# Optimization experiments

Hardware: AMD Instinct MI355X
Metric: run time of the kernel (lower is better)

## Reference

```python
import jax, jax.numpy as jnp
import numpy as np

P_TOP = 0.1          # fraction of brightest pixels for atmosphere
LEC_K = 3            # local-extremum conv kernel size (w=3 in forward)
HID = 64             # hidden channels of stand-in Net


def _conv2d(x, w, pad):
    return jax.lax.conv_general_dilated(
        x, w, window_strides=(1, 1), padding=[(pad, pad), (pad, pad)],
        dimension_numbers=("NCHW", "OIHW", "NCHW"))


def _lec_weights(k, dtype):
    # LocalExtremumConv.init_weights: all +/-1/k^2 with +/-1 at the center
    base = jnp.full((1, 1, k, k), 1.0 / (k * k), dtype=dtype)
    base = base.at[0, 0, k // 2, k // 2].set(1.0)
    return -base, base  # (min_weights, max_weights)


def setup_inputs() -> dict:
    key = jax.random.key(0)
    ks = jax.random.split(key, 8)
    B, C, H, W = 8, 3, 512, 512
    x = jax.random.uniform(ks[0], (B, C, H, W), dtype=jnp.float32)
    s1 = 1.0 / np.sqrt(C * 9)
    s2 = 1.0 / np.sqrt(HID * 9)
    return {
        "x": x,
        "net_w1": jax.random.normal(ks[1], (HID, C, 3, 3), jnp.float32) * s1,
        "net_b1": jnp.zeros((HID,), jnp.float32),
        "net_w2": jax.random.normal(ks[2], (C, HID, 3, 3), jnp.float32) * s2,
        "net_b2": jnp.zeros((C,), jnp.float32),
        "color_w": jax.random.normal(ks[3], (3, 3), jnp.float32) * (1.0 / np.sqrt(3)),
        "color_b": jnp.zeros((3,), jnp.float32),
        "conv_w": jax.random.normal(ks[4], (4, 3, 1, 1), jnp.float32) * (1.0 / np.sqrt(3)),
        "conv_b": jnp.zeros((4,), jnp.float32),
    }


def reference(x, net_w1, net_b1, net_w2, net_b2, color_w, color_b, conv_w, conv_b):
    B, C, H, W = x.shape
    # --- stand-in Net: 3->64->3 conv enhancement, sigmoid output ---
    h = jax.nn.relu(_conv2d(x, net_w1, 1) + net_b1[None, :, None, None])
    img_high = jax.nn.sigmoid(_conv2d(h, net_w2, 1) + net_b2[None, :, None, None])
    # --- stand-in Color_pred: GAP -> linear -> sigmoid -> (B,3,1,1) gain ---
    color = jax.nn.sigmoid(x.mean(axis=(2, 3)) @ color_w.T + color_b)
    img_high = img_high * color[:, :, None, None]
    # --- 1x1 conv -> split K (1ch), Bias (3ch); residual correction ---
    feat = _conv2d(img_high, conv_w, 0) + conv_b[None, :, None, None]
    K, Bt = feat[:, 0:1], feat[:, 1:4]
    x_out = K * x - Bt + x
    # --- illumination channel: reflect pad + channel min/max + LEC convs ---
    pad = LEC_K // 2
    xp = jnp.pad(x_out, ((0, 0), (0, 0), (pad, pad), (pad, pad)), mode="reflect")
    x_max = xp.max(axis=1, keepdims=True)
    _, max_w = _lec_weights(LEC_K, x.dtype)
    bright = jax.nn.relu(_conv2d(x_max, max_w, 0))  # (B,1,H,W)
    # --- atmosphere: top-p% brightest pixels, gather + mean ---
    # NOTE: faithful to torch images.view(B,-1,C) on NCHW (layout-scrambled)
    flat_img = x_out.reshape(B, H * W, C)
    flat_bright = bright.reshape(B, H * W)
    num_pixels = int(P_TOP * H * W)
    _, idx = jax.lax.top_k(flat_bright, num_pixels)          # (B, num_pixels)
    picked = jnp.take_along_axis(flat_img, idx[:, :, None], axis=1)
    A = picked.mean(axis=1)                                   # (B, C)
    return (x_out, A)
```

## Files before the change

### kernel.cpp

```cpp
#include <hip/hip_runtime.h>
#include <hip/hip_bf16.h>

#define Hn 512
#define Wn 512
#define HWn (512 * 512)
#define KTOP 26214

#define HBS 70
#define HBROW (18 * HBS)

typedef __attribute__((ext_vector_type(8))) short frag_ab;
typedef __attribute__((ext_vector_type(4))) float frag_cd;

__device__ __forceinline__ float sigf(float z) { return 1.0f / (1.0f + __expf(-z)); }

__device__ __forceinline__ short f2bf(float f) {
  unsigned u = __float_as_uint(f);
  u += 0x7FFFu + ((u >> 16) & 1u);
  return (short)(u >> 16);
}

__device__ __forceinline__ unsigned aload(const unsigned* p) {
  return __hip_atomic_load(p, __ATOMIC_RELAXED, __HIP_MEMORY_SCOPE_AGENT);
}

__global__ __launch_bounds__(256) void k_means(
    const float* __restrict__ x, float* __restrict__ means, unsigned* __restrict__ doneCnt,
    const float* __restrict__ w1, const float* __restrict__ b1, const float* __restrict__ w2,
    const float* __restrict__ cw, const float* __restrict__ cb,
    short* __restrict__ w1A, short* __restrict__ w2A, int* __restrict__ kbTab,
    float* __restrict__ colorG)
{
  const int tid = threadIdx.x;
  __shared__ int lastS;
  int bc = blockIdx.x >> 5;
  int slice = blockIdx.x & 31;
  const float4* p = (const float4*)(x + bc * HWn + slice * 8192);
  float s = 0.f;
  for (int i = tid; i < 2048; i += 256) { float4 v = p[i]; s += v.x + v.y + v.z + v.w; }
  for (int off = 32; off > 0; off >>= 1) s += __shfl_down(s, off);
  if ((tid & 63) == 0) atomicAdd(&means[bc], s);
  __syncthreads();
  if (tid == 0) {
    unsigned tk = __hip_atomic_fetch_add(doneCnt, 1u, __ATOMIC_RELAXED, __HIP_MEMORY_SCOPE_AGENT);
    lastS = (tk == 767);
  }
  __syncthreads();
  if (!lastS) return;

  {
    int chunk = tid >> 6, lane = tid & 63;
    int m = lane & 15, q = lane >> 4;
    for (int j = 0; j < 8; ++j) {
      int k = q * 8 + j;
      float v = (k < 27) ? w1[(chunk * 16 + m) * 27 + k] : 0.f;
      w1A[tid * 8 + j] = f2bf(v);
    }
  }
  if (tid < 64) {
    int q = tid >> 4;
    for (int j = 0; j < 8; ++j) {
      int k = q * 8 + j;
      int kk = (k < 27) ? k : (k - 27);
      int ic = kk / 9; int r = kk - ic * 9;
      kbTab[tid * 8 + j] = (ic * 240 + (r / 3) * 20 + (r % 3)) * 2;
    }
  }
  for (int i = tid; i < 384; i += 256) {
    int step = i >> 6, lane = i & 63;
    int m = lane & 15, q = lane >> 4;
    int dx = step >> 1, half = step & 1;
    int dy = m / 3, oc = m - dy * 3;
    for (int j = 0; j < 8; ++j) {
      int ch = half * 32 + q * 8 + j;
      float v = (m < 9) ? w2[oc * 576 + ch * 9 + dy * 3 + dx] : 0.f;
      w2A[i * 8 + j] = f2bf(v);
    }
  }
  if (tid < 24) {
    int b = tid / 3, oc = tid % 3;
    float z = cb[oc];
    for (int j = 0; j < 3; ++j)
      z += (atomicAdd(&means[b * 3 + j], 0.f) * (1.0f / (float)HWn)) * cw[oc * 3 + j];
    colorG[tid] = sigf(z);
  }
}

__global__ __launch_bounds__(256, 6) void k_fused(
    const float* __restrict__ x, const float* __restrict__ b1,
    const float* __restrict__ b2, const float* __restrict__ convw, const float* __restrict__ convb,
    const short* __restrict__ w1Ag, const short* __restrict__ w2Ag,
    const int* __restrict__ kbTab,
    const float* __restrict__ colorG, float* __restrict__ out, float* __restrict__ Mb)
{
  __shared__ __align__(16) unsigned short xs[720];
  __shared__ __align__(16) unsigned short hb[180 * HBS];
  __shared__ float bs[64];
  __shared__ float b2s[3], colorS[3], cwS[12], cbS[4];

  const int tid = threadIdx.x;
  const int wid = tid >> 6, lane = tid & 63;
  const int n = lane & 15, q = lane >> 4;
  const int tx0 = blockIdx.x * 16, ty0 = blockIdx.y * 8;
  const int b = blockIdx.z;
  const bool inter = (blockIdx.x - 1u) < 30u && (blockIdx.y - 1u) < 62u;

  if (tid < 180) {
    int c = tid / 60, rem = tid - c * 60;
    int yy = rem / 5, xq = (rem - yy * 5) * 4;
    int gy = ty0 - 2 + yy, gx0 = tx0 - 2 + xq;
    const float* rp = x + (b * 3 + c) * HWn + (gy << 9) + gx0;
    float v0, v1, v2, v3;
    if (inter) {
      v0 = rp[0]; v1 = rp[1]; v2 = rp[2]; v3 = rp[3];
    } else {
      bool rowok = (unsigned)gy < 512u;
      v0 = (rowok && (unsigned)(gx0 + 0) < 512u) ? rp[0] : 0.f;
      v1 = (rowok && (unsigned)(gx0 + 1) < 512u) ? rp[1] : 0.f;
      v2 = (rowok && (unsigned)(gx0 + 2) < 512u) ? rp[2] : 0.f;
      v3 = (rowok && (unsigned)(gx0 + 3) < 512u) ? rp[3] : 0.f;
    }
    __hip_bfloat162 c01 = __float22bfloat162_rn(make_float2(v0, v1));
    __hip_bfloat162 c23 = __float22bfloat162_rn(make_float2(v2, v3));
    uint2 v2w; v2w.x = *(unsigned*)&c01; v2w.y = *(unsigned*)&c23;
    *(uint2*)(xs + c * 240 + yy * 20 + xq) = v2w;
  }
  if (tid < 64) bs[tid] = b1[tid];
  if (tid < 3)  b2s[tid] = b2[tid];
  if (tid < 3)  colorS[tid] = colorG[b * 3 + tid];
  if (tid < 12) cwS[tid] = convw[tid];
  if (tid < 4)  cbS[tid] = convb[tid];

  frag_ab w1f[4];
#pragma unroll
  for (int ck = 0; ck < 4; ++ck) w1f[ck] = *(const frag_ab*)(w1Ag + (ck * 64 + lane) * 8);

  int kb[8];
  {
    const int4* kp = (const int4*)(kbTab + lane * 8);
    int4 ka = kp[0], kc = kp[1];
    kb[0] = ka.x; kb[1] = ka.y; kb[2] = ka.z; kb[3] = ka.w;
    kb[4] = kc.x; kb[5] = kc.y; kb[6] = kc.z; kb[7] = kc.w;
  }
  __syncthreads();

  float biasr[4][4];
#pragma unroll
  for (int ck = 0; ck < 4; ++ck)
#pragma unroll
    for (int r = 0; r < 4; ++r) biasr[ck][r] = bs[ck * 16 + q * 4 + r];

  if (inter) {
    for (int g = wid; g < 12; g += 4) {
      int pt = g * 16 + n;
      int ptc = (pt < 180) ? pt : 179;
      int pty = (ptc * 3641) >> 16;
      int ptx = ptc - pty * 18;
      int baseB = (pty * 20 + ptx) * 2;
      frag_ab B;
#pragma unroll
      for (int j = 0; j < 8; ++j)
        B[j] = *(const short*)((const char*)xs + baseB + kb[j]);
#pragma unroll
      for (int ck = 0; ck < 4; ++ck) {
        frag_cd D = {biasr[ck][0], biasr[ck][1], biasr[ck][2], biasr[ck][3]};
        D = __builtin_amdgcn_mfma_f32_16x16x32_bf16(w1f[ck], B, D, 0, 0, 0);
        float2 p01 = make_float2(fmaxf(D[0], 0.f), fmaxf(D[1], 0.f));
        float2 p23 = make_float2(fmaxf(D[2], 0.f), fmaxf(D[3], 0.f));
        __hip_bfloat162 c01 = __float22bfloat162_rn(p01);
        __hip_bfloat162 c23 = __float22bfloat162_rn(p23);
        uint2 v2; v2.x = *(unsigned*)&c01; v2.y = *(unsigned*)&c23;
        *(uint2*)(hb + ptc * HBS + ck * 16 + q * 4) = v2;
      }
    }
  } else {
    for (int g = wid; g < 12; g += 4) {
      int pt = g * 16 + n;
      int ptc = (pt < 180) ? pt : 179;
      int pty = (ptc * 3641) >> 16;
      int ptx = ptc - pty * 18;
      int baseB = (pty * 20 + ptx) * 2;
      int gy = ty0 - 1 + pty, gx = tx0 - 1 + ptx;
      bool valid = (unsigned)gy < 512u && (unsigned)gx < 512u;
      frag_ab B;
#pragma unroll
      for (int j = 0; j < 8; ++j)
        B[j] = *(const short*)((const char*)xs + baseB + kb[j]);
#pragma unroll
      for (int ck = 0; ck < 4; ++ck) {
        frag_cd D = {biasr[ck][0], biasr[ck][1], biasr[ck][2], biasr[ck][3]};
        D = __builtin_amdgcn_mfma_f32_16x16x32_bf16(w1f[ck], B, D, 0, 0, 0);
        float2 p01 = make_float2(fmaxf(D[0], 0.f), fmaxf(D[1], 0.f));
        float2 p23 = make_float2(fmaxf(D[2], 0.f), fmaxf(D[3], 0.f));
        __hip_bfloat162 c01 = __float22bfloat162_rn(p01);
        __hip_bfloat162 c23 = __float22bfloat162_rn(p23);
        unsigned lo = valid ? *(unsigned*)&c01 : 0u;
        unsigned hi = valid ? *(unsigned*)&c23 : 0u;
        uint2 v2; v2.x = lo; v2.y = hi;
        *(uint2*)(hb + ptc * HBS + ck * 16 + q * 4) = v2;
      }
    }
  }

  frag_ab w2f[6];
#pragma unroll
  for (int i = 0; i < 6; ++i) w2f[i] = *(const frag_ab*)(w2Ag + (i * 64 + lane) * 8);
  __syncthreads();

  for (int r = wid; r < 10; r += 4) {
    frag_cd acc = {0.f, 0.f, 0.f, 0.f};
#pragma unroll
    for (int i = 0; i < 6; ++i) {
      int dx = i >> 1;
      int chb = (i & 1) * 64 + q * 16;
      frag_ab Bf = *(const frag_ab*)((const char*)hb + (r * 18 + n + dx) * (HBS * 2) + chb);
      acc = __builtin_amdgcn_mfma_f32_16x16x32_bf16(w2f[i], Bf, acc, 0, 0, 0);
    }
    float* dp = (float*)(hb + r * HBROW) + n * 10 + q * 4;
    if (q < 2) {
      *(float2*)dp = make_float2(acc[0], acc[1]);
      *(float2*)(dp + 2) = make_float2(acc[2], acc[3]);
    } else if (q == 2) {
      dp[0] = acc[0];
    }
  }
  __syncthreads();

  if (tid < 128) {
    int y = tid >> 4, xcol = tid & 15;
    float a0 = b2s[0], a1 = b2s[1], a2 = b2s[2];
#pragma unroll
    for (int dy = 0; dy < 3; ++dy) {
      const float* dp = (const float*)(hb + (y + dy) * HBROW) + xcol * 10 + dy * 3;
      a0 += dp[0]; a1 += dp[1]; a2 += dp[2];
    }
    float ih0 = colorS[0] * sigf(a0);
    float ih1 = colorS[1] * sigf(a1);
    float ih2 = colorS[2] * sigf(a2);
    float Kv = cwS[0] * ih0 + cwS[1]  * ih1 + cwS[2]  * ih2 + cbS[0];
    float f1 = cwS[3] * ih0 + cwS[4]  * ih1 + cwS[5]  * ih2 + cbS[1];
    float f2 = cwS[6] * ih0 + cwS[7]  * ih1 + cwS[8]  * ih2 + cbS[2];
    float f3 = cwS[9] * ih0 + cwS[10] * ih1 + cwS[11] * ih2 + cbS[3];
    float xc0 = __bfloat162float(*(const __hip_bfloat16*)&xs[0 * 240 + (y + 2) * 20 + (xcol + 2)]);
    float xc1 = __bfloat162float(*(const __hip_bfloat16*)&xs[1 * 240 + (y + 2) * 20 + (xcol + 2)]);
    float xc2 = __bfloat162float(*(const __hip_bfloat16*)&xs[2 * 240 + (y + 2) * 20 + (xcol + 2)]);
    int oi = ((ty0 + y) << 9) + (tx0 + xcol);
    float o0 = Kv * xc0 - f1 + xc0;
    float o1 = Kv * xc1 - f2 + xc1;
    float o2 = Kv * xc2 - f3 + xc2;
    out[(b * 3 + 0) * HWn + oi] = o0;
    out[(b * 3 + 1) * HWn + oi] = o1;
    out[(b * 3 + 2) * HWn + oi] = o2;
    Mb[b * HWn + oi] = fmaxf(fmaxf(o0, o1), o2);
  }
}

__device__ __forceinline__ void softBarrier(unsigned* ctr, unsigned target) {
  __syncthreads();
  if (threadIdx.x == 0) {
    __hip_atomic_fetch_add(ctr, 1u, __ATOMIC_RELAXED, __HIP_MEMORY_SCOPE_AGENT);
    while (__hip_atomic_load(ctr, __ATOMIC_RELAXED, __HIP_MEMORY_SCOPE_AGENT) < target)
      __builtin_amdgcn_s_sleep(2);
  }
  __syncthreads();
}

__device__ void sel256(const unsigned* __restrict__ h, unsigned kneed,
                       unsigned* sm, unsigned* oBin, unsigned* oAbove)
{
  const int t = threadIdx.x;
  sm[t] = aload(&h[t]);
  __syncthreads();
  for (int d = 1; d < 256; d <<= 1) {
    unsigned add = (t + d < 256) ? sm[t + d] : 0u;
    __syncthreads();
    sm[t] += add;
    __syncthreads();
  }
  unsigned mine = sm[t];
  unsigned nxt = (t < 255) ? sm[t + 1] : 0u;
  if (mine >= kneed && nxt < kneed) { *oBin = (unsigned)t; *oAbove = nxt; }
  __syncthreads();
}

__device__ void sel4096(const unsigned* __restrict__ h, unsigned kneed,
                        unsigned* sm, unsigned* oBin, unsigned* oAbove)
{
  const int t = threadIdx.x;
  unsigned loc[16]; unsigned sum = 0;
#pragma unroll
  for (int i = 0; i < 16; ++i) { loc[i] = aload(&h[t * 16 + i]); sum += loc[i]; }
  sm[t] = sum;
  __syncthreads();
  for (int d = 1; d < 256; d <<= 1) {
    unsigned add = (t + d < 256) ? sm[t + d] : 0u;
    __syncthreads();
    sm[t] += add;
    __syncthreads();
  }
  unsigned mine = sm[t];
  unsigned nxt = (t < 255) ? sm[t + 1] : 0u;
  if (mine >= kneed && nxt < kneed) {
    unsigned acc = nxt;
    for (int i = 15; i >= 0; --i) {
      unsigned c = loc[i];
      if (acc + c >= kneed) { *oBin = (unsigned)(t * 16 + i); *oAbove = acc; break; }
      acc += c;
    }
  }
  __syncthreads();
}

__global__ __launch_bounds__(256) void k_tail(
    const float* __restrict__ Mbuf, const float* __restrict__ outv,
    unsigned* __restrict__ h1, unsigned* __restrict__ h12,
    unsigned* __restrict__ eqTaken, float* __restrict__ Asum,
    unsigned* __restrict__ barCtr, unsigned* __restrict__ doneCnt, float* __restrict__ outA)
{
  __shared__ __align__(16) char smem[20640];
  __shared__ __align__(16) float brightS[4096];
  __shared__ unsigned sB1, sA1, sB2, sA2;
  __shared__ float red[4][3];
  __shared__ int lastA;

  float (*xm)[516] = (float (*)[516])smem;
  unsigned* hh = (unsigned*)smem;
  unsigned* sm = (unsigned*)(smem + 16384);

  const int tid = threadIdx.x;
  const int b = blockIdx.x >> 6, strip = blockIdx.x & 63;
  const int y0 = strip * 8;
  const float* mp = Mbuf + b * HWn;
  const float* op = outv + b * 3 * HWn;
  unsigned* bar = barCtr + b * 48;

  for (int idx = tid; idx < 1280; idx += 256) {
    int r = idx >> 7, seg = idx & 127;
    int gy = y0 - 1 + r; gy = (gy < 0) ? -gy : (gy > 511 ? 1022 - gy : gy);
    int c0 = seg * 4;
    float4 v = *(const float4*)(mp + (gy << 9) + c0);
    xm[r][c0 + 1] = v.x;
    xm[r][c0 + 2] = v.y;
    xm[r][c0 + 3] = v.z;
    xm[r][c0 + 4] = v.w;
  }
  if (tid < 20) {
    int r = tid >> 1, side = tid & 1;
    int gy = y0 - 1 + r; gy = (gy < 0) ? -gy : (gy > 511 ? 1022 - gy : gy);
    int gx = side ? 510 : 1;
    xm[r][side ? 513 : 0] = mp[(gy << 9) + gx];
  }
  __syncthreads();
  {
    const int row = tid >> 5, cl = tid & 31;
#pragma unroll 4
    for (int i = 0; i < 16; ++i) {
      int c = cl + (i << 5);
      float s0 = xm[row][c]     + xm[row][c + 1]     + xm[row][c + 2];
      float s1 = xm[row + 1][c] + xm[row + 1][c + 1] + xm[row + 1][c + 2];
      float s2 = xm[row + 2][c] + xm[row + 2][c + 1] + xm[row + 2][c + 2];
      float s = (s0 + s1 + s2) * (1.f / 9.f) + xm[row + 1][c + 1] * (8.f / 9.f);
      s = fmaxf(s, 0.f);
      brightS[(row << 9) + c] = s;
    }
  }
  __syncthreads();

  hh[tid] = 0;
  __syncthreads();
  {
    unsigned cb0 = 0x100, cc0 = 0, cb1 = 0x100, cc1 = 0;
    const float4* bp4 = (const float4*)brightS;
#pragma unroll
    for (int it = 0; it < 4; ++it) {
      float4 v = bp4[it * 256 + tid];
      unsigned bins[4] = { __float_as_uint(v.x) >> 24, __float_as_uint(v.y) >> 24,
                           __float_as_uint(v.z) >> 24, __float_as_uint(v.w) >> 24 };
#pragma unroll
      for (int j = 0; j < 4; ++j) {
        unsigned bb = bins[j];
        if (bb == cb0) ++cc0;
        else if (bb == cb1) ++cc1;
        else if (!cc0) { cb0 = bb; cc0 = 1; }
        else if (!cc1) { cb1 = bb; cc1 = 1; }
        else atomicAdd(&hh[bb], 1u);
      }
    }
    if (cc0) atomicAdd(&hh[cb0], cc0);
    if (cc1) atomicAdd(&hh[cb1], cc1);
  }
  __syncthreads();
  if (hh[tid]) atomicAdd(&h1[(b << 8) + tid], hh[tid]);
  softBarrier(bar, 64);

  sel256(h1 + (b << 8), KTOP, sm, &sB1, &sA1);
  for (int i = tid; i < 4096; i += 256) hh[i] = 0;
  __syncthreads();
  const float4* bp = (const float4*)brightS;
  const unsigned sb1 = sB1;
#pragma unroll
  for (int it = 0; it < 4; ++it) {
    float4 v = bp[it * 256 + tid];
    unsigned u0 = __float_as_uint(v.x), u1 = __float_as_uint(v.y);
    unsigned u2 = __float_as_uint(v.z), u3 = __float_as_uint(v.w);
    if ((u0 >> 24) == sb1) atomicAdd(&hh[(u0 >> 12) & 0xFFFu], 1u);
    if ((u1 >> 24) == sb1) atomicAdd(&hh[(u1 >> 12) & 0xFFFu], 1u);
    if ((u2 >> 24) == sb1) atomicAdd(&hh[(u2 >> 12) & 0xFFFu], 1u);
    if ((u3 >> 24) == sb1) atomicAdd(&hh[(u3 >> 12) & 0xFFFu], 1u);
  }
  __syncthreads();
  for (int i = tid; i < 4096; i += 256)
    if (hh[i]) atomicAdd(&h12[(b << 12) + i], hh[i]);
  if (tid == 0) { sB2 = 0xFFFu; sA2 = 0u; }
  softBarrier(bar + 16, 64);

  sel4096(h12 + (b << 12), KTOP - sA1, sm, &sB2, &sA2);
  const unsigned T20 = (sB1 << 12) | sB2;
  const unsigned ne = KTOP - sA1 - sA2;
  float v0 = 0.f, v1 = 0.f, v2 = 0.f;
  for (int it = 0; it < 16; ++it) {
    int li = it * 256 + tid;
    int pix = (y0 << 9) + li;
    unsigned u20 = __float_as_uint(brightS[li]) >> 12;
    bool take = u20 > T20;
    if (u20 == T20) {
      if (aload(&eqTaken[b * 16]) < ne) {
        unsigned old = atomicAdd(&eqTaken[b * 16], 1u);
        take = old < ne;
      }
    }
    if (take) {
      v0 += op[3 * pix];
      v1 += op[3 * pix + 1];
      v2 += op[3 * pix + 2];
    }
  }
  for (int off = 32; off > 0; off >>= 1) {
    v0 += __shfl_down(v0, off);
    v1 += __shfl_down(v1, off);
    v2 += __shfl_down(v2, off);
  }
  int w = tid >> 6;
  if ((tid & 63) == 0) { red[w][0] = v0; red[w][1] = v1; red[w][2] = v2; }
  __syncthreads();
  if (tid == 0) {
    atomicAdd(&Asum[b * 3 + 0], red[0][0] + red[1][0] + red[2][0] + red[3][0]);
    atomicAdd(&Asum[b * 3 + 1], red[0][1] + red[1][1] + red[2][1] + red[3][1]);
    atomicAdd(&Asum[b * 3 + 2], red[0][2] + red[1][2] + red[2][2] + red[3][2]);
  }
  __syncthreads();
  if (tid == 0) {
    unsigned tk = __hip_atomic_fetch_add(doneCnt, 1u, __ATOMIC_RELAXED, __HIP_MEMORY_SCOPE_AGENT);
    lastA = (tk == 511);
  }
  __syncthreads();
  if (lastA && tid < 24)
    outA[3 * HWn * 8 + tid] = atomicAdd(&Asum[tid], 0.f) * (1.0f / (float)KTOP);
}

extern "C" void kernel_launch(void* const* d_in, const int* in_sizes, int n_in,
                              void* d_out, int out_size, void* d_ws, size_t ws_size,
                              hipStream_t stream)
{
  const float* x     = (const float*)d_in[0];
  const float* w1    = (const float*)d_in[1];
  const float* b1    = (const float*)d_in[2];
  const float* w2    = (const float*)d_in[3];
  const float* b2    = (const float*)d_in[4];
  const float* cw    = (const float*)d_in[5];
  const float* cb    = (const float*)d_in[6];
  const float* convw = (const float*)d_in[7];
  const float* convb = (const float*)d_in[8];
  float* out = (float*)d_out;
  char* ws = (char*)d_ws;

  float*    Mbuf      = (float*)(ws);
  unsigned* h1        = (unsigned*)(ws + 8388608);
  unsigned* h12       = (unsigned*)(ws + 8396800);
  float*    Asum      = (float*)(ws + 8658944);
  unsigned* eqTaken   = (unsigned*)(ws + 8659040);
  float*    means     = (float*)(ws + 8659552);
  unsigned* meansDone = (unsigned*)(ws + 8659648);
  unsigned* accumDone = (unsigned*)(ws + 8659680);
  unsigned* barCtr    = (unsigned*)(ws + 8659712);
  short*    w1Ag      = (short*)(ws + 8661248);
  short*    w2Ag      = (short*)(ws + 8665344);
  float*    colorG    = (float*)(ws + 8683776);
  int*      kbTab     = (int*)(ws + 8683904);

  hipMemsetAsync(ws + 8388608, 0, 8661248 - 8388608, stream);

  k_means<<<768, 256, 0, stream>>>(x, means, meansDone, w1, b1, w2, cw, cb, w1Ag, w2Ag, kbTab, colorG);
  k_fused<<<dim3(32, 64, 8), 256, 0, stream>>>(x, b1, b2, convw, convb, w1Ag, w2Ag, kbTab, colorG, out, Mbuf);
  k_tail<<<512, 256, 0, stream>>>(Mbuf, out, h1, h12, eqTaken, Asum, barCtr, accumDone, out);
}
```

Before: 244.0 us.

## Loop batch inside fused conv kernel to amortize per-block setup

Removes the batch dimension from the fused kernel grid, so each block walks all 8 images serially and reuses per-tile setup across them. That setup covers weight fragment loads, bias staging, index and mask precompute, and the color gains for all batches. The separate interior and boundary paths are merged into one predicated path. Launch bounds drop from 6 to 4 waves per SIMD, and the grid shrinks eightfold to 2048 blocks. This costs parallelism and latency hiding, and adds extra barriers per batch iteration.

After: 248.6 us. No clear change (+1.9%).

```diff
diff --git a/kernel.cpp b/kernel.cpp
--- a/kernel.cpp
+++ b/kernel.cpp
@@ -86,7 +86,7 @@
   }
 }
 
-__global__ __launch_bounds__(256, 6) void k_fused(
+__global__ __launch_bounds__(256, 4) void k_fused(
     const float* __restrict__ x, const float* __restrict__ b1,
     const float* __restrict__ b2, const float* __restrict__ convw, const float* __restrict__ convb,
     const short* __restrict__ w1Ag, const short* __restrict__ w2Ag,
@@ -96,44 +96,44 @@
   __shared__ __align__(16) unsigned short xs[720];
   __shared__ __align__(16) unsigned short hb[180 * HBS];
   __shared__ float bs[64];
-  __shared__ float b2s[3], colorS[3], cwS[12], cbS[4];
+  __shared__ float b2s[3], colorAll[24], cwS[12], cbS[4];
 
   const int tid = threadIdx.x;
   const int wid = tid >> 6, lane = tid & 63;
   const int n = lane & 15, q = lane >> 4;
   const int tx0 = blockIdx.x * 16, ty0 = blockIdx.y * 8;
-  const int b = blockIdx.z;
   const bool inter = (blockIdx.x - 1u) < 30u && (blockIdx.y - 1u) < 62u;
 
-  if (tid < 180) {
+  if (tid < 64) bs[tid] = b1[tid];
+  if (tid < 3)  b2s[tid] = b2[tid];
+  if (tid < 24) colorAll[tid] = colorG[tid];
+  if (tid < 12) cwS[tid] = convw[tid];
+  if (tid < 4)  cbS[tid] = convb[tid];
+
+  bool sOn = tid < 180;
+  int rowBase = 0, chanOff = 0;
+  unsigned short* sDst = xs;
+  bool ok0 = false, ok1 = false, ok2 = false, ok3 = false;
+  if (sOn) {
     int c = tid / 60, rem = tid - c * 60;
     int yy = rem / 5, xq = (rem - yy * 5) * 4;
     int gy = ty0 - 2 + yy, gx0 = tx0 - 2 + xq;
-    const float* rp = x + (b * 3 + c) * HWn + (gy << 9) + gx0;
-    float v0, v1, v2, v3;
-    if (inter) {
-      v0 = rp[0]; v1 = rp[1]; v2 = rp[2]; v3 = rp[3];
-    } else {
-      bool rowok = (unsigned)gy < 512u;
-      v0 = (rowok && (unsigned)(gx0 + 0) < 512u) ? rp[0] : 0.f;
-      v1 = (rowok && (unsigned)(gx0 + 1) < 512u) ? rp[1] : 0.f;
-      v2 = (rowok && (unsigned)(gx0 + 2) < 512u) ? rp[2] : 0.f;
-      v3 = (rowok && (unsigned)(gx0 + 3) < 512u) ? rp[3] : 0.f;
-    }
-    __hip_bfloat162 c01 = __float22bfloat162_rn(make_float2(v0, v1));
-    __hip_bfloat162 c23 = __float22bfloat162_rn(make_float2(v2, v3));
-    uint2 v2w; v2w.x = *(unsigned*)&c01; v2w.y = *(unsigned*)&c23;
-    *(uint2*)(xs + c * 240 + yy * 20 + xq) = v2w;
-  }
-  if (tid < 64) bs[tid] = b1[tid];
-  if (tid < 3)  b2s[tid] = b2[tid];
-  if (tid < 3)  colorS[tid] = colorG[b * 3 + tid];
-  if (tid < 12) cwS[tid] = convw[tid];
-  if (tid < 4)  cbS[tid] = convb[tid];
+    rowBase = (gy << 9) + gx0;
+    chanOff = c * HWn;
+    sDst = xs + c * 240 + yy * 20 + xq;
+    bool rowok = (unsigned)gy < 512u;
+    ok0 = inter || (rowok && (unsigned)(gx0 + 0) < 512u);
+    ok1 = inter || (rowok && (unsigned)(gx0 + 1) < 512u);
+    ok2 = inter || (rowok && (unsigned)(gx0 + 2) < 512u);
+    ok3 = inter || (rowok && (unsigned)(gx0 + 3) < 512u);
+  }
 
   frag_ab w1f[4];
 #pragma unroll
   for (int ck = 0; ck < 4; ++ck) w1f[ck] = *(const frag_ab*)(w1Ag + (ck * 64 + lane) * 8);
+  frag_ab w2f[6];
+#pragma unroll
+  for (int i = 0; i < 6; ++i) w2f[i] = *(const frag_ab*)(w2Ag + (i * 64 + lane) * 8);
 
   int kb[8];
   {
@@ -142,6 +142,20 @@
     kb[0] = ka.x; kb[1] = ka.y; kb[2] = ka.z; kb[3] = ka.w;
     kb[4] = kc.x; kb[5] = kc.y; kb[6] = kc.z; kb[7] = kc.w;
   }
+
+  int baseA[3], stA[3];
+  bool keepA[3];
+#pragma unroll
+  for (int u = 0; u < 3; ++u) {
+    int pt = (wid + u * 4) * 16 + n;
+    int ptc = (pt < 180) ? pt : 179;
+    int pty = (ptc * 3641) >> 16;
+    int ptx = ptc - pty * 18;
+    baseA[u] = (pty * 20 + ptx) * 2;
+    stA[u] = ptc * HBS + q * 4;
+    int gy = ty0 - 1 + pty, gx = tx0 - 1 + ptx;
+    keepA[u] = inter || ((unsigned)gy < 512u && (unsigned)gx < 512u);
+  }
   __syncthreads();
 
   float biasr[4][4];
@@ -150,17 +164,27 @@
 #pragma unroll
     for (int r = 0; r < 4; ++r) biasr[ck][r] = bs[ck * 16 + q * 4 + r];
 
-  if (inter) {
-    for (int g = wid; g < 12; g += 4) {
-      int pt = g * 16 + n;
-      int ptc = (pt < 180) ? pt : 179;
-      int pty = (ptc * 3641) >> 16;
-      int ptx = ptc - pty * 18;
-      int baseB = (pty * 20 + ptx) * 2;
+#pragma unroll 1
+  for (int b = 0; b < 8; ++b) {
+    if (sOn) {
+      const float* rp = x + b * 3 * HWn + chanOff + rowBase;
+      float v0 = ok0 ? rp[0] : 0.f;
+      float v1 = ok1 ? rp[1] : 0.f;
+      float v2 = ok2 ? rp[2] : 0.f;
+      float v3 = ok3 ? rp[3] : 0.f;
+      __hip_bfloat162 c01 = __float22bfloat162_rn(make_float2(v0, v1));
+      __hip_bfloat162 c23 = __float22bfloat162_rn(make_float2(v2, v3));
+      uint2 v2w; v2w.x = *(unsigned*)&c01; v2w.y = *(unsigned*)&c23;
+      *(uint2*)sDst = v2w;
+    }
+    __syncthreads();
+
+#pragma unroll
+    for (int u = 0; u < 3; ++u) {
       frag_ab B;
 #pragma unroll
       for (int j = 0; j < 8; ++j)
-        B[j] = *(const short*)((const char*)xs + baseB + kb[j]);
+        B[j] = *(const short*)((const char*)xs + baseA[u] + kb[j]);
 #pragma unroll
       for (int ck = 0; ck < 4; ++ck) {
         frag_cd D = {biasr[ck][0], biasr[ck][1], biasr[ck][2], biasr[ck][3]};
@@ -169,89 +193,61 @@
         float2 p23 = make_float2(fmaxf(D[2], 0.f), fmaxf(D[3], 0.f));
         __hip_bfloat162 c01 = __float22bfloat162_rn(p01);
         __hip_bfloat162 c23 = __float22bfloat162_rn(p23);
-        uint2 v2; v2.x = *(unsigned*)&c01; v2.y = *(unsigned*)&c23;
-        *(uint2*)(hb + ptc * HBS + ck * 16 + q * 4) = v2;
-      }
-    }
-  } else {
-    for (int g = wid; g < 12; g += 4) {
-      int pt = g * 16 + n;
-      int ptc = (pt < 180) ? pt : 179;
-      int pty = (ptc * 3641) >> 16;
-      int ptx = ptc - pty * 18;
-      int baseB = (pty * 20 + ptx) * 2;
-      int gy = ty0 - 1 + pty, gx = tx0 - 1 + ptx;
-      bool valid = (unsigned)gy < 512u && (unsigned)gx < 512u;
-      frag_ab B;
-#pragma unroll
-      for (int j = 0; j < 8; ++j)
-        B[j] = *(const short*)((const char*)xs + baseB + kb[j]);
-#pragma unroll
-      for (int ck = 0; ck < 4; ++ck) {
-        frag_cd D = {biasr[ck][0], biasr[ck][1], biasr[ck][2], biasr[ck][3]};
-        D = __builtin_amdgcn_mfma_f32_16x16x32_bf16(w1f[ck], B, D, 0, 0, 0);
-        float2 p01 = make_float2(fmaxf(D[0], 0.f), fmaxf(D[1], 0.f));
-        float2 p23 = make_float2(fmaxf(D[2], 0.f), fmaxf(D[3], 0.f));
-        __hip_bfloat162 c01 = __float22bfloat162_rn(p01);
-        __hip_bfloat162 c23 = __float22bfloat162_rn(p23);
-        unsigned lo = valid ? *(unsigned*)&c01 : 0u;
-        unsigned hi = valid ? *(unsigned*)&c23 : 0u;
+        unsigned lo = keepA[u] ? *(unsigned*)&c01 : 0u;
+        unsigned hi = keepA[u] ? *(unsigned*)&c23 : 0u;
         uint2 v2; v2.x = lo; v2.y = hi;
-        *(uint2*)(hb + ptc * HBS + ck * 16 + q * 4) = v2;
-      }
-    }
-  }
-
-  frag_ab w2f[6];
-#pragma unroll
-  for (int i = 0; i < 6; ++i) w2f[i] = *(const frag_ab*)(w2Ag + (i * 64 + lane) * 8);
-  __syncthreads();
-
-  for (int r = wid; r < 10; r += 4) {
-    frag_cd acc = {0.f, 0.f, 0.f, 0.f};
-#pragma unroll
-    for (int i = 0; i < 6; ++i) {
-      int dx = i >> 1;
-      int chb = (i & 1) * 64 + q * 16;
-      frag_ab Bf = *(const frag_ab*)((const char*)hb + (r * 18 + n + dx) * (HBS * 2) + chb);
-      acc = __builtin_amdgcn_mfma_f32_16x16x32_bf16(w2f[i], Bf, acc, 0, 0, 0);
-    }
-    float* dp = (float*)(hb + r * HBROW) + n * 10 + q * 4;
-    if (q < 2) {
-      *(float2*)dp = make_float2(acc[0], acc[1]);
-      *(float2*)(dp + 2) = make_float2(acc[2], acc[3]);
-    } else if (q == 2) {
-      dp[0] = acc[0];
-    }
-  }
-  __syncthreads();
-
-  if (tid < 128) {
-    int y = tid >> 4, xcol = tid & 15;
-    float a0 = b2s[0], a1 = b2s[1], a2 = b2s[2];
-#pragma unroll
-    for (int dy = 0; dy < 3; ++dy) {
-      const float* dp = (const float*)(hb + (y + dy) * HBROW) + xcol * 10 + dy * 3;
-      a0 += dp[0]; a1 += dp[1]; a2 += dp[2];
-    }
-    float ih0 = colorS[0] * sigf(a0);
-    float ih1 = colorS[1] * sigf(a1);
-    float ih2 = colorS[2] * sigf(a2);
-    float Kv = cwS[0] * ih0 + cwS[1]  * ih1 + cwS[2]  * ih2 + cbS[0];
-    float f1 = cwS[3] * ih0 + cwS[4]  * ih1 + cwS[5]  * ih2 + cbS[1];
-    float f2 = cwS[6] * ih0 + cwS[7]  * ih1 + cwS[8]  * ih2 + cbS[2];
-    float f3 = cwS[9] * ih0 + cwS[10] * ih1 + cwS[11] * ih2 + cbS[3];
-    float xc0 = __bfloat162float(*(const __hip_bfloat16*)&xs[0 * 240 + (y + 2) * 20 + (xcol + 2)]);
-    float xc1 = __bfloat162float(*(const __hip_bfloat16*)&xs[1 * 240 + (y + 2) * 20 + (xcol + 2)]);
-    float xc2 = __bfloat162float(*(const __hip_bfloat16*)&xs[2 * 240 + (y + 2) * 20 + (xcol + 2)]);
-    int oi = ((ty0 + y) << 9) + (tx0 + xcol);
-    float o0 = Kv * xc0 - f1 + xc0;
-    float o1 = Kv * xc1 - f2 + xc1;
-    float o2 = Kv * xc2 - f3 + xc2;
-    out[(b * 3 + 0) * HWn + oi] = o0;
-    out[(b * 3 + 1) * HWn + oi] = o1;
-    out[(b * 3 + 2) * HWn + oi] = o2;
-    Mb[b * HWn + oi] = fmaxf(fmaxf(o0, o1), o2);
+        *(uint2*)(hb + stA[u] + ck * 16) = v2;
+      }
+    }
+    __syncthreads();
+
+    for (int r = wid; r < 10; r += 4) {
+      frag_cd acc = {0.f, 0.f, 0.f, 0.f};
+#pragma unroll
+      for (int i = 0; i < 6; ++i) {
+        int dx = i >> 1;
+        int chb = (i & 1) * 64 + q * 16;
+        frag_ab Bf = *(const frag_ab*)((const char*)hb + (r * 18 + n + dx) * (HBS * 2) + chb);
+        acc = __builtin_amdgcn_mfma_f32_16x16x32_bf16(w2f[i], Bf, acc, 0, 0, 0);
+      }
+      float* dp = (float*)(hb + r * HBROW) + n * 10 + q * 4;
+      if (q < 2) {
+        *(float2*)dp = make_float2(acc[0], acc[1]);
+        *(float2*)(dp + 2) = make_float2(acc[2], acc[3]);
+      } else if (q == 2) {
+        dp[0] = acc[0];
+      }
+    }
+    __syncthreads();
+
+    if (tid < 128) {
+      int y = tid >> 4, xcol = tid & 15;
+      float a0 = b2s[0], a1 = b2s[1], a2 = b2s[2];
+#pragma unroll
+      for (int dy = 0; dy < 3; ++dy) {
+        const float* dp = (const float*)(hb + (y + dy) * HBROW) + xcol * 10 + dy * 3;
+        a0 += dp[0]; a1 += dp[1]; a2 += dp[2];
+      }
+      float ih0 = colorAll[b * 3 + 0] * sigf(a0);
+      float ih1 = colorAll[b * 3 + 1] * sigf(a1);
+      float ih2 = colorAll[b * 3 + 2] * sigf(a2);
+      float Kv = cwS[0] * ih0 + cwS[1]  * ih1 + cwS[2]  * ih2 + cbS[0];
+      float f1 = cwS[3] * ih0 + cwS[4]  * ih1 + cwS[5]  * ih2 + cbS[1];
+      float f2 = cwS[6] * ih0 + cwS[7]  * ih1 + cwS[8]  * ih2 + cbS[2];
+      float f3 = cwS[9] * ih0 + cwS[10] * ih1 + cwS[11] * ih2 + cbS[3];
+      float xc0 = __bfloat162float(*(const __hip_bfloat16*)&xs[0 * 240 + (y + 2) * 20 + (xcol + 2)]);
+      float xc1 = __bfloat162float(*(const __hip_bfloat16*)&xs[1 * 240 + (y + 2) * 20 + (xcol + 2)]);
+      float xc2 = __bfloat162float(*(const __hip_bfloat16*)&xs[2 * 240 + (y + 2) * 20 + (xcol + 2)]);
+      int oi = ((ty0 + y) << 9) + (tx0 + xcol);
+      float o0 = Kv * xc0 - f1 + xc0;
+      float o1 = Kv * xc1 - f2 + xc1;
+      float o2 = Kv * xc2 - f3 + xc2;
+      out[(b * 3 + 0) * HWn + oi] = o0;
+      out[(b * 3 + 1) * HWn + oi] = o1;
+      out[(b * 3 + 2) * HWn + oi] = o2;
+      Mb[b * HWn + oi] = fmaxf(fmaxf(o0, o1), o2);
+    }
+    __syncthreads();
   }
 }
 
@@ -491,6 +487,6 @@
   hipMemsetAsync(ws + 8388608, 0, 8661248 - 8388608, stream);
 
   k_means<<<768, 256, 0, stream>>>(x, means, meansDone, w1, b1, w2, cw, cb, w1Ag, w2Ag, kbTab, colorG);
-  k_fused<<<dim3(32, 64, 8), 256, 0, stream>>>(x, b1, b2, convw, convb, w1Ag, w2Ag, kbTab, colorG, out, Mbuf);
+  k_fused<<<dim3(32, 64), 256, 0, stream>>>(x, b1, b2, convw, convb, w1Ag, w2Ag, kbTab, colorG, out, Mbuf);
   k_tail<<<512, 256, 0, stream>>>(Mbuf, out, h1, h12, eqTaken, Asum, barCtr, accumDone, out);
 }
```
